# Kernel tuning notes

Measured on AMD Instinct MI355X. Metric: run time of the kernel, lower is better.

Reference implementation:

```python
import jax, jax.numpy as jnp
import numpy as np

N_NODES = 100000
N_EDGES = 1600000
GENE_DIM = 256
HID = 128
NUM_CLASSES = 2
BN_EPS = 1e-5


def setup_inputs() -> dict:
    key = jax.random.key(0)
    ks = jax.random.split(key, 24)
    g = lambda k, shape, scale: (jax.random.normal(k, shape, dtype=jnp.float32) * scale)
    inp = {
        "x": g(ks[0], (N_NODES, GENE_DIM), 1.0),
        "edge_index": jax.random.randint(ks[1], (2, N_EDGES), 0, N_NODES, dtype=jnp.int64),
        # GCNConv weights (glorot-ish scale) and biases
        "W1": g(ks[2], (GENE_DIM, HID), 1.0 / np.sqrt(GENE_DIM)), "b1": jnp.zeros((HID,), jnp.float32),
        "W2": g(ks[3], (HID, 2 * HID), 1.0 / np.sqrt(HID)), "b2": jnp.zeros((2 * HID,), jnp.float32),
        "W3": g(ks[4], (2 * HID, HID), 1.0 / np.sqrt(2 * HID)), "b3": jnp.zeros((HID,), jnp.float32),
        "W4": g(ks[5], (HID, HID // 2), 1.0 / np.sqrt(HID)), "b4": jnp.zeros((HID // 2,), jnp.float32),
        "Wc": g(ks[6], (HID // 2, NUM_CLASSES), 1.0 / np.sqrt(HID // 2)), "bc": jnp.zeros((NUM_CLASSES,), jnp.float32),
        # BatchNorm affine params
        "g1": jnp.ones((HID,), jnp.float32), "be1": jnp.zeros((HID,), jnp.float32),
        "g2": jnp.ones((2 * HID,), jnp.float32), "be2": jnp.zeros((2 * HID,), jnp.float32),
        "g3": jnp.ones((HID,), jnp.float32), "be3": jnp.zeros((HID,), jnp.float32),
        "g4": jnp.ones((HID // 2,), jnp.float32), "be4": jnp.zeros((HID // 2,), jnp.float32),
    }
    return inp


def _batchnorm(h, gamma, beta):
    # training-mode BatchNorm1d: per-feature batch stats (biased variance)
    mean = h.mean(axis=0)
    var = ((h - mean) ** 2).mean(axis=0)
    return gamma * (h - mean) * jax.lax.rsqrt(var + BN_EPS) + beta


def _gcn_conv(h, W, b, src, dst, norm, n):
    # PyG GCNConv: linear transform, then sym-normalized aggregation over
    # edges (self-loops already included in src/dst/norm), then bias.
    m = h @ W                                   # [n, d_out]
    msg = m[src] * norm[:, None]                # [E+n, d_out] gather
    agg = jax.ops.segment_sum(msg, dst, num_segments=n)  # scatter-add
    return agg + b


def reference(x, edge_index, W1, b1, W2, b2, W3, b3, W4, b4, Wc, bc,
              g1, be1, g2, be2, g3, be3, g4, be4):
    n = x.shape[0]
    loop = jnp.arange(n, dtype=edge_index.dtype)
    src = jnp.concatenate([edge_index[0], loop])  # add self-loops
    dst = jnp.concatenate([edge_index[1], loop])
    deg = jax.ops.segment_sum(jnp.ones_like(dst, dtype=x.dtype), dst, num_segments=n)
    dinv = jax.lax.rsqrt(jnp.maximum(deg, 1.0))
    norm = dinv[src] * dinv[dst]                  # D^-1/2 (A+I) D^-1/2

    h = jax.nn.relu(_gcn_conv(x, W1, b1, src, dst, norm, n))
    h = _batchnorm(h, g1, be1)
    h = jax.nn.relu(_gcn_conv(h, W2, b2, src, dst, norm, n))
    h = _batchnorm(h, g2, be2)
    h = jax.nn.relu(_gcn_conv(h, W3, b3, src, dst, norm, n))
    h = _batchnorm(h, g3, be3)
    out4 = jax.nn.relu(_gcn_conv(h, W4, b4, src, dst, norm, n))
    bn4 = _batchnorm(out4, g4, be4)
    logits = bn4 @ Wc + bc
    return (logits, out4, bn4)
```

## Files before the change

### kernel.cpp

```cpp
#include <hip/hip_runtime.h>
#include <hip/hip_bf16.h>

#define N_NODES 100000
#define N_EDGES 1600000
#define NB ((N_NODES + 255) / 256)
#define CHUNK 16384
#define NBLK ((N_EDGES + CHUNK - 1) / CHUNK)
#define NSHADOW 32
#define WCB 416
#define SB 512

typedef short sh8 __attribute__((ext_vector_type(8)));
typedef float f32x4 __attribute__((ext_vector_type(4)));

__device__ __forceinline__ float bf2f(unsigned short s) {
    return __uint_as_float(((unsigned int)s) << 16);
}
__device__ __forceinline__ unsigned short f2bf(float f) {
    unsigned int u = __float_as_uint(f);
    unsigned int r = (u + 0x7FFFu + ((u >> 16) & 1u)) >> 16;
    return (unsigned short)r;
}
__device__ __forceinline__ float blo(unsigned int u) { return __uint_as_float(u << 16); }
__device__ __forceinline__ float bhi(unsigned int u) { return __uint_as_float(u & 0xffff0000u); }


__global__ __launch_bounds__(256) void k_hist(const int* __restrict__ ei, int* __restrict__ histG) {
    __shared__ int hist[NB];
    int blk = blockIdx.x, t = threadIdx.x;
    for (int b = t; b < NB; b += 256) hist[b] = 0;
    __syncthreads();
    int e0 = blk * CHUNK;
    int e1 = min(e0 + CHUNK, N_EDGES);
    for (int e = e0 + t; e < e1; e += 256) atomicAdd(&hist[ei[N_EDGES + e] >> 8], 1);
    __syncthreads();
    for (int b = t; b < NB; b += 256) histG[b * NBLK + blk] = hist[b];
}

__global__ __launch_bounds__(128) void k_scanrow(int* __restrict__ histG, int* __restrict__ rowsum) {
    __shared__ int sm[128];
    int b = blockIdx.x, t = threadIdx.x;
    int v = (t < NBLK) ? histG[b * NBLK + t] : 0;
    sm[t] = v; __syncthreads();
    for (int d = 1; d < 128; d <<= 1) {
        int add = (t >= d) ? sm[t - d] : 0;
        __syncthreads(); sm[t] += add; __syncthreads();
    }
    if (t < NBLK) histG[b * NBLK + t] = sm[t] - v;
    if (t == 127) rowsum[b] = sm[127];
}

__global__ __launch_bounds__(512) void k_scanbkt(const int* __restrict__ rowsum, int* __restrict__ rowbase) {
    __shared__ int sm[512];
    int t = threadIdx.x;
    int v = (t < NB) ? rowsum[t] : 0;
    sm[t] = v; __syncthreads();
    for (int d = 1; d < 512; d <<= 1) {
        int add = (t >= d) ? sm[t - d] : 0;
        __syncthreads(); sm[t] += add; __syncthreads();
    }
    if (t <= NB) rowbase[t] = sm[t] - v;
}

__global__ __launch_bounds__(256) void k_part(const int* __restrict__ ei, const int* __restrict__ histG,
                                              const int* __restrict__ rowbase, unsigned* __restrict__ pairs) {
    __shared__ int cur[NB];
    int blk = blockIdx.x, t = threadIdx.x;
    for (int b = t; b < NB; b += 256) cur[b] = rowbase[b] + histG[b * NBLK + blk];
    __syncthreads();
    int e0 = blk * CHUNK;
    int e1 = min(e0 + CHUNK, N_EDGES);
    for (int e = e0 + t; e < e1; e += 256) {
        int s = ei[e], d = ei[N_EDGES + e];
        int pos = atomicAdd(&cur[d >> 8], 1);
        pairs[pos] = ((unsigned)s << 8) | (unsigned)(d & 255);
    }
}

__global__ __launch_bounds__(256) void k_bsort(const unsigned* __restrict__ pairs, const int* __restrict__ rowbase,
                                               int* __restrict__ col, int* __restrict__ basep,
                                               int* __restrict__ deg, float* __restrict__ dinv,
                                               float* __restrict__ sdeg) {
    __shared__ int cnt[256];
    __shared__ int sm[256];
    __shared__ int cur[256];
    int b = blockIdx.x, t = threadIdx.x;
    int base = rowbase[b], end = rowbase[b + 1];
    cnt[t] = 0; __syncthreads();
    for (int e = base + t; e < end; e += 256) atomicAdd(&cnt[pairs[e] & 255], 1);
    __syncthreads();
    int v = cnt[t];
    sm[t] = v; __syncthreads();
    for (int d = 1; d < 256; d <<= 1) {
        int add = (t >= d) ? sm[t - d] : 0;
        __syncthreads(); sm[t] += add; __syncthreads();
    }
    int excl = sm[t] - v;
    cur[t] = excl;
    int gd = (b << 8) + t;
    if (gd < N_NODES) {
        basep[gd] = base + excl;
        deg[gd] = v;
        dinv[gd] = rsqrtf((float)(v + 1));
        sdeg[gd] = sqrtf((float)(v + 1));
    }
    __syncthreads();
    for (int e = base + t; e < end; e += 256) {
        unsigned p = pairs[e];
        int pos = atomicAdd(&cur[p & 255], 1);
        col[base + pos] = (int)(p >> 8);
    }
}


__global__ __launch_bounds__(256) void k_wsvec(const float* __restrict__ W1, const float* __restrict__ W2,
                                               const float* __restrict__ W3, const float* __restrict__ W4,
                                               unsigned short* __restrict__ Wt1, unsigned short* __restrict__ Wt2,
                                               unsigned short* __restrict__ Wt3, unsigned short* __restrict__ Wt4,
                                               const int* __restrict__ col, const int* __restrict__ basep,
                                               const int* __restrict__ deg, const float* __restrict__ dinv,
                                               float* __restrict__ svec) {
    if (blockIdx.x < WCB) {
        int idx = blockIdx.x * 256 + threadIdx.x;
        const float* W; unsigned short* Wt; int K, N, base;
        if (idx < 32768)       { W = W1; Wt = Wt1; K = 256; N = 128; base = 0; }
        else if (idx < 65536)  { W = W2; Wt = Wt2; K = 128; N = 256; base = 32768; }
        else if (idx < 98304)  { W = W3; Wt = Wt3; K = 256; N = 128; base = 65536; }
        else if (idx < 106496) { W = W4; Wt = Wt4; K = 128; N = 64;  base = 98304; }
        else return;
        int li = idx - base;
        int n = li / K, k = li - n * K;
        Wt[li] = f2bf(W[(size_t)k * N + n]);
        return;
    }
    int sb = blockIdx.x - WCB;
    int w = (sb * 256 + threadIdx.x) >> 6;
    if (w >= N_NODES) return;
    int lane = threadIdx.x & 63;
    int start = basep[w], cnt = deg[w];
    float s = 0.f;
    for (int j = lane; j < cnt; j += 64) s += dinv[col[start + j]];
#pragma unroll
    for (int off = 32; off; off >>= 1) s += __shfl_down(s, off, 64);
    if (lane == 0) { float di = dinv[w]; svec[w] = di * (s + di); }
}


__global__ __launch_bounds__(256) void k_bnred(const float* __restrict__ arena, float* __restrict__ dst) {
    int f = blockIdx.x * 256 + threadIdx.x;
    float s = 0.f;
#pragma unroll
    for (int i = 0; i < NSHADOW; ++i) s += arena[i * 512 + f];
    dst[f] = s;
}


template <int D, bool INF32, bool RESCALE>
__device__ __forceinline__ void bnstats_body(int bid, int gridN, const void* __restrict__ h,
                                             const float* __restrict__ sdeg, float* __restrict__ arena) {
    constexpr int VEC = INF32 ? 4 : 8;
    constexpr int TPR = D / VEC;
    constexpr int RPB = 256 / TPR;
    const int tid = threadIdx.x;
    const int rg = tid / TPR;
    const int oc = tid % TPR;
    const int fb = oc * VEC;

    float s1[VEC], s2[VEC];
#pragma unroll
    for (int k = 0; k < VEC; ++k) { s1[k] = 0.f; s2[k] = 0.f; }

    for (int r = bid * RPB + rg; r < N_NODES; r += gridN * RPB) {
        float rs = 1.f;
        if constexpr (RESCALE) rs = sdeg[r];
        if constexpr (INF32) {
            float4 v = *(const float4*)((const float*)h + (size_t)r * D + fb);
            float vv[4] = {v.x, v.y, v.z, v.w};
#pragma unroll
            for (int k = 0; k < 4; ++k) {
                float val = vv[k];
                if constexpr (RESCALE) val *= rs;
                s1[k] += val; s2[k] += val * val;
            }
        } else {
            uint4 u = *(const uint4*)((const unsigned short*)h + (size_t)r * D + fb);
            unsigned uu[4] = {u.x, u.y, u.z, u.w};
#pragma unroll
            for (int k = 0; k < 4; ++k) {
                float v0 = blo(uu[k]), v1 = bhi(uu[k]);
                if constexpr (RESCALE) { v0 *= rs; v1 *= rs; }
                s1[2 * k] += v0;     s2[2 * k] += v0 * v0;
                s1[2 * k + 1] += v1; s2[2 * k + 1] += v1 * v1;
            }
        }
    }

    __shared__ float red[2][D];
    for (int i = tid; i < 2 * D; i += 256) ((float*)red)[i] = 0.f;
    __syncthreads();
#pragma unroll
    for (int k = 0; k < VEC; ++k) {
        atomicAdd(&red[0][fb + k], s1[k]);
        atomicAdd(&red[1][fb + k], s2[k]);
    }
    __syncthreads();
    float* slot = arena + ((bid & (NSHADOW - 1)) << 9);
    for (int i = tid; i < 2 * D; i += 256) {
        int f = (i < D) ? i : (256 + i - D);
        float v = (i < D) ? red[0][i] : red[1][i - D];
        atomicAdd(&slot[f], v);
    }
}

template <int D, bool INF32, bool RESCALE>
__global__ __launch_bounds__(256) void k_bnstats(const void* __restrict__ h,
                                                 const float* __restrict__ sdeg,
                                                 float* __restrict__ arena) {
    bnstats_body<D, INF32, RESCALE>(blockIdx.x, gridDim.x, h, sdeg, arena);
}


template <int D, bool PRE, bool OUTF32, bool OUTSCALE>
__device__ __forceinline__ void agg_body(int bid, const unsigned short* __restrict__ m,
                                         const int* __restrict__ col,
                                         const int* __restrict__ basep,
                                         const int* __restrict__ deg,
                                         const float* __restrict__ dinv,
                                         const float* __restrict__ bias,
                                         void* __restrict__ out) {
    constexpr int VPL = D / 64;
    const int w = (bid * 256 + threadIdx.x) >> 6;
    if (w >= N_NODES) return;
    const int lane = threadIdx.x & 63;
    const int fo = lane * VPL;
    const unsigned short* mfo = m + fo;
    float acc[VPL];
#pragma unroll
    for (int k = 0; k < VPL; ++k) acc[k] = 0.f;

    int start = basep[w], cnt = deg[w];
    int j = 0;
    for (; j + 8 <= cnt; j += 8) {
        int sx[8];
#pragma unroll
        for (int i = 0; i < 8; ++i) sx[i] = col[start + j + i];
        if constexpr (VPL == 2) {
            unsigned u[8];
#pragma unroll
            for (int i = 0; i < 8; ++i) u[i] = *(const unsigned*)(mfo + (size_t)sx[i] * D);
#pragma unroll
            for (int i = 0; i < 8; ++i) { acc[0] += blo(u[i]); acc[1] += bhi(u[i]); }
        } else {
            float v[8];
#pragma unroll
            for (int i = 0; i < 8; ++i) v[i] = bf2f(mfo[(size_t)sx[i] * D]);
#pragma unroll
            for (int i = 0; i < 8; ++i) acc[0] += v[i];
        }
    }
    for (; j < cnt; ++j) {
        int s0 = col[start + j];
        if constexpr (VPL == 2) {
            unsigned u0 = *(const unsigned*)(mfo + (size_t)s0 * D);
            acc[0] += blo(u0); acc[1] += bhi(u0);
        } else {
            acc[0] += bf2f(mfo[(size_t)s0 * D]);
        }
    }
    if constexpr (VPL == 2) {
        unsigned u0 = *(const unsigned*)(mfo + (size_t)w * D);
        acc[0] += blo(u0); acc[1] += bhi(u0);
    } else {
        acc[0] += bf2f(mfo[(size_t)w * D]);
    }

    float di = dinv[w];
    float o[VPL];
    if constexpr (PRE) {
#pragma unroll
        for (int k = 0; k < VPL; ++k) o[k] = acc[k] * di;
    } else {
#pragma unroll
        for (int k = 0; k < VPL; ++k) {
            o[k] = fmaxf(acc[k] * di + bias[fo + k], 0.f);
            if constexpr (OUTSCALE) o[k] *= di;
        }
    }

    if constexpr (OUTF32) {
        float* of = (float*)out;
#pragma unroll
        for (int k = 0; k < VPL; ++k) of[(size_t)w * D + fo + k] = o[k];
    } else {
        unsigned short* ob = (unsigned short*)out + (size_t)w * D + fo;
        if constexpr (VPL == 2) {
            unsigned int u = (unsigned)f2bf(o[0]) | ((unsigned)f2bf(o[1]) << 16);
            *(unsigned int*)ob = u;
        } else {
            ob[0] = f2bf(o[0]);
        }
    }
}

template <int D, bool PRE, bool OUTF32, bool OUTSCALE>
__global__ __launch_bounds__(256) void k_agg(const unsigned short* __restrict__ m,
                                             const int* __restrict__ col,
                                             const int* __restrict__ basep,
                                             const int* __restrict__ deg,
                                             const float* __restrict__ dinv,
                                             const float* __restrict__ bias,
                                             void* __restrict__ out) {
    agg_body<D, PRE, OUTF32, OUTSCALE>(blockIdx.x, m, col, basep, deg, dinv, bias, out);
}


__global__ __launch_bounds__(256) void k_aggpre_stats(const unsigned short* __restrict__ hb,
                                                      const int* __restrict__ col,
                                                      const int* __restrict__ basep,
                                                      const int* __restrict__ deg,
                                                      const float* __restrict__ dinv,
                                                      const float* __restrict__ sdeg,
                                                      unsigned short* __restrict__ mb,
                                                      float* __restrict__ arena) {
    if (blockIdx.x < SB) {
        bnstats_body<128, false, true>(blockIdx.x, SB, hb, sdeg, arena);
    } else {
        agg_body<128, true, false, false>(blockIdx.x - SB, hb, col, basep, deg, dinv, nullptr, mb);
    }
}


template <bool OUTF32>
__global__ __launch_bounds__(256) void k_agg64(const unsigned short* __restrict__ m,
                                               const int* __restrict__ col,
                                               const int* __restrict__ basep,
                                               const int* __restrict__ deg,
                                               const float* __restrict__ dinv,
                                               const float* __restrict__ bias,
                                               void* __restrict__ out) {
    const int w = (blockIdx.x * 256 + threadIdx.x) >> 5;
    if (w >= N_NODES) return;
    const int hl = threadIdx.x & 31;
    const int fo = hl * 2;
    const unsigned short* mfo = m + fo;
    float acc0 = 0.f, acc1 = 0.f;

    int start = basep[w], cnt = deg[w];
    int j = 0;
    for (; j + 8 <= cnt; j += 8) {
        int sx[8];
#pragma unroll
        for (int i = 0; i < 8; ++i) sx[i] = col[start + j + i];
        unsigned u[8];
#pragma unroll
        for (int i = 0; i < 8; ++i) u[i] = *(const unsigned*)(mfo + (size_t)sx[i] * 64);
#pragma unroll
        for (int i = 0; i < 8; ++i) { acc0 += blo(u[i]); acc1 += bhi(u[i]); }
    }
    for (; j < cnt; ++j) {
        int s0 = col[start + j];
        unsigned u0 = *(const unsigned*)(mfo + (size_t)s0 * 64);
        acc0 += blo(u0); acc1 += bhi(u0);
    }
    {
        unsigned u0 = *(const unsigned*)(mfo + (size_t)w * 64);
        acc0 += blo(u0); acc1 += bhi(u0);
    }

    float di = dinv[w];
    float o0 = fmaxf(acc0 * di + bias[fo], 0.f);
    float o1 = fmaxf(acc1 * di + bias[fo + 1], 0.f);

    if constexpr (OUTF32) {
        *(float2*)((float*)out + (size_t)w * 64 + fo) = make_float2(o0, o1);
    } else {
        unsigned u = (unsigned)f2bf(o0) | ((unsigned)f2bf(o1) << 16);
        *(unsigned*)((unsigned short*)out + (size_t)w * 64 + fo) = u;
    }
}


template <int BM, int BN, int AMODE, bool BIASRELU, bool DSCALE>
__global__ __launch_bounds__(512) void k_gemm4(const void* __restrict__ Ain,
                                               const unsigned short* __restrict__ Wt,
                                               const float* __restrict__ arena,
                                               const float* __restrict__ gamma,
                                               const float* __restrict__ beta,
                                               const float* __restrict__ svec,
                                               const float* __restrict__ bias,
                                               const float* __restrict__ dinv,
                                               unsigned short* __restrict__ Mout,
                                               int K, int NTOT) {
    constexpr int BK = 64;
    constexpr int LDA = 72;
    constexpr int AP = BM / 64;
    constexpr int BP = BN / 64;
    constexpr int MF = BM / 32;
    constexpr int NF = BN / 64;
    __shared__ unsigned short As[BM * LDA];
    __shared__ unsigned short Bs[BN * LDA];
    __shared__ float ss_sc[256];
    __shared__ float ss_sh[256];
    const int tid = threadIdx.x;
    const int lane = tid & 63;
    const int wv = tid >> 6;
    const int wm = wv >> 2;
    const int wn = wv & 3;
    const int row0 = blockIdx.x * BM;
    const int col0 = blockIdx.y * BN;

    if constexpr (AMODE >= 1) {
        for (int f = tid; f < K; f += 512) {
            float s1 = 0.f, s2 = 0.f;
#pragma unroll
            for (int s = 0; s < NSHADOW; ++s) {
                s1 += arena[s * 512 + f];
                s2 += arena[s * 512 + 256 + f];
            }
            float mean = s1 * (1.f / N_NODES);
            float var = s2 * (1.f / N_NODES) - mean * mean;
            float inv = rsqrtf(var + 1e-5f);
            float sc = gamma[f] * inv;
            ss_sc[f] = sc;
            ss_sh[f] = beta[f] - mean * sc;
        }
        __syncthreads();
    }

    const int sr = tid >> 3;
    const int scc = (tid & 7) * 8;

    float4 fa[AP][2];
    uint4 ua[AP];
    uint4 ub[BP];
    float sv[AP];

    auto LOAD = [&](int k0) {
#pragma unroll
        for (int p = 0; p < AP; ++p) {
            int gr = row0 + p * 64 + sr;
            if constexpr (AMODE == 0) {
                const float* Af = (const float*)Ain;
                fa[p][0] = make_float4(0.f, 0.f, 0.f, 0.f); fa[p][1] = fa[p][0];
                if (gr < N_NODES) {
                    const float* p0 = Af + (size_t)gr * K + k0 + scc;
                    fa[p][0] = *(const float4*)p0;
                    fa[p][1] = *(const float4*)(p0 + 4);
                }
            } else {
                const unsigned short* Ab = (const unsigned short*)Ain;
                ua[p] = make_uint4(0, 0, 0, 0);
                if (gr < N_NODES) ua[p] = *(const uint4*)(Ab + (size_t)gr * K + k0 + scc);
                if constexpr (AMODE == 2) sv[p] = (gr < N_NODES) ? svec[gr] : 0.f;
            }
        }
#pragma unroll
        for (int p = 0; p < BP; ++p)
            ub[p] = *(const uint4*)(Wt + (size_t)(col0 + p * 64 + sr) * K + k0 + scc);
    };

    auto WRITE = [&](int k0) {
#pragma unroll
        for (int p = 0; p < AP; ++p) {
            alignas(16) unsigned short tmp[8];
            if constexpr (AMODE == 0) {
                tmp[0] = f2bf(fa[p][0].x); tmp[1] = f2bf(fa[p][0].y);
                tmp[2] = f2bf(fa[p][0].z); tmp[3] = f2bf(fa[p][0].w);
                tmp[4] = f2bf(fa[p][1].x); tmp[5] = f2bf(fa[p][1].y);
                tmp[6] = f2bf(fa[p][1].z); tmp[7] = f2bf(fa[p][1].w);
            } else {
                const unsigned short* pr = (const unsigned short*)&ua[p];
#pragma unroll
                for (int q = 0; q < 8; ++q) {
                    float sc = ss_sc[k0 + scc + q];
                    float sh = ss_sh[k0 + scc + q];
                    float val;
                    if constexpr (AMODE == 2) val = bf2f(pr[q]) * sc + sh * sv[p];
                    else val = bf2f(pr[q]) * sc + sh;
                    tmp[q] = f2bf(val);
                }
            }
            *(uint4*)&As[(p * 64 + sr) * LDA + scc] = *(const uint4*)tmp;
        }
#pragma unroll
        for (int p = 0; p < BP; ++p) *(uint4*)&Bs[(p * 64 + sr) * LDA + scc] = ub[p];
    };

    f32x4 acc[MF][NF];
#pragma unroll
    for (int i = 0; i < MF; ++i)
#pragma unroll
        for (int j = 0; j < NF; ++j)
#pragma unroll
            for (int r = 0; r < 4; ++r) acc[i][j][r] = 0.f;

    LOAD(0);
    WRITE(0);
    __syncthreads();
    const int nk = K / BK;
    for (int kt = 1; kt <= nk; ++kt) {
        if (kt < nk) LOAD(kt * BK);
#pragma unroll
        for (int ks = 0; ks < 2; ++ks) {
            sh8 af[MF], bfr[NF];
#pragma unroll
            for (int i = 0; i < MF; ++i)
                af[i] = *(const sh8*)&As[(wm * (BM / 2) + i * 16 + (lane & 15)) * LDA + ks * 32 + (lane >> 4) * 8];
#pragma unroll
            for (int j = 0; j < NF; ++j)
                bfr[j] = *(const sh8*)&Bs[(wn * NF * 16 + j * 16 + (lane & 15)) * LDA + ks * 32 + (lane >> 4) * 8];
#pragma unroll
            for (int i = 0; i < MF; ++i)
#pragma unroll
                for (int j = 0; j < NF; ++j)
                    acc[i][j] = __builtin_amdgcn_mfma_f32_16x16x32_bf16(af[i], bfr[j], acc[i][j], 0, 0, 0);
        }
        __syncthreads();
        if (kt < nk) {
            WRITE(kt * BK);
            __syncthreads();
        }
    }

#pragma unroll
    for (int i = 0; i < MF; ++i) {
#pragma unroll
        for (int r = 0; r < 4; ++r) {
            int grow = row0 + wm * (BM / 2) + i * 16 + (lane >> 4) * 4 + r;
            if (grow >= N_NODES) continue;
            float rsc = 1.f;
            if constexpr (DSCALE) rsc = dinv[grow];
#pragma unroll
            for (int j = 0; j < NF; ++j) {
                int gcol = col0 + wn * NF * 16 + j * 16 + (lane & 15);
                float v = acc[i][j][r];
                if constexpr (BIASRELU) v = fmaxf(v + bias[gcol], 0.f);
                if constexpr (DSCALE) v *= rsc;
                Mout[(size_t)grow * NTOT + gcol] = f2bf(v);
            }
        }
    }
}


__global__ __launch_bounds__(256) void k_bnlog(const float* __restrict__ out4, const float* __restrict__ sums,
                                               const float* __restrict__ gamma, const float* __restrict__ beta,
                                               const float* __restrict__ Wc, const float* __restrict__ bc,
                                               float* __restrict__ bn4, float* __restrict__ logits) {
    int gw = (blockIdx.x * 256 + threadIdx.x) >> 6;
    if (gw >= N_NODES) return;
    int f = threadIdx.x & 63;
    float mean = sums[f] * (1.f / N_NODES);
    float var = sums[256 + f] * (1.f / N_NODES) - mean * mean;
    float inv = rsqrtf(var + 1e-5f);
    float sc = gamma[f] * inv;
    float sh = beta[f] - mean * sc;
    float v = out4[(size_t)gw * 64 + f];
    float bn = v * sc + sh;
    bn4[(size_t)gw * 64 + f] = bn;
    float a0 = bn * Wc[2 * f];
    float a1 = bn * Wc[2 * f + 1];
#pragma unroll
    for (int off = 32; off; off >>= 1) {
        a0 += __shfl_down(a0, off, 64);
        a1 += __shfl_down(a1, off, 64);
    }
    if (f == 0) {
        logits[2 * gw] = a0 + bc[0];
        logits[2 * gw + 1] = a1 + bc[1];
    }
}


extern "C" void kernel_launch(void* const* d_in, const int* in_sizes, int n_in,
                              void* d_out, int out_size, void* d_ws, size_t ws_size,
                              hipStream_t stream) {
    const float* x  = (const float*)d_in[0];
    const int* ei   = (const int*)d_in[1];
    const float* W1 = (const float*)d_in[2];  const float* b1  = (const float*)d_in[3];
    const float* W2 = (const float*)d_in[4];  const float* b2  = (const float*)d_in[5];
    const float* W3 = (const float*)d_in[6];  const float* b3  = (const float*)d_in[7];
    const float* W4 = (const float*)d_in[8];  const float* b4  = (const float*)d_in[9];
    const float* Wc = (const float*)d_in[10]; const float* bc  = (const float*)d_in[11];
    const float* g1 = (const float*)d_in[12]; const float* be1 = (const float*)d_in[13];
    const float* g2 = (const float*)d_in[14]; const float* be2 = (const float*)d_in[15];
    const float* g3 = (const float*)d_in[16]; const float* be3 = (const float*)d_in[17];
    const float* g4 = (const float*)d_in[18]; const float* be4 = (const float*)d_in[19];

    char* wsb = (char*)d_ws;
    size_t off = 0;
    auto alloc = [&](size_t bytes) -> void* {
        void* p = wsb + off;
        off = (off + bytes + 511) & ~(size_t)511;
        return p;
    };
    int* deg     = (int*)alloc((size_t)N_NODES * 4);
    int* basep   = (int*)alloc((size_t)N_NODES * 4);
    float* dinv  = (float*)alloc((size_t)N_NODES * 4);
    float* sdeg  = (float*)alloc((size_t)N_NODES * 4);
    float* svec  = (float*)alloc((size_t)N_NODES * 4);
    int* col     = (int*)alloc((size_t)N_EDGES * 4);
    unsigned* pairs = (unsigned*)alloc((size_t)N_EDGES * 4);
    int* histG   = (int*)alloc((size_t)NB * NBLK * 4);
    int* rowsum  = (int*)alloc((size_t)NB * 4);
    int* rowbase = (int*)alloc((size_t)(NB + 1) * 4);
    float* sums4  = (float*)alloc(512 * 4);
    float* shadow = (float*)alloc((size_t)4 * NSHADOW * 512 * 4);
    unsigned short* Wt1 = (unsigned short*)alloc((size_t)256 * 128 * 2);
    unsigned short* Wt2 = (unsigned short*)alloc((size_t)128 * 256 * 2);
    unsigned short* Wt3 = (unsigned short*)alloc((size_t)256 * 128 * 2);
    unsigned short* Wt4 = (unsigned short*)alloc((size_t)128 * 64 * 2);
    unsigned short* mb = (unsigned short*)alloc((size_t)N_NODES * 128 * 2);
    unsigned short* hb = (unsigned short*)alloc((size_t)N_NODES * 256 * 2);

    float* arena1 = shadow;
    float* arena2 = shadow + NSHADOW * 512;
    float* arena3 = shadow + 2 * NSHADOW * 512;
    float* arena4 = shadow + 3 * NSHADOW * 512;

    float* outLogits = (float*)d_out;
    float* out4 = outLogits + (size_t)N_NODES * 2;
    float* bn4  = out4 + (size_t)N_NODES * 64;

    hipMemsetAsync(sums4, 0, 512 * 4 + (size_t)4 * NSHADOW * 512 * 4, stream);

    k_hist<<<NBLK, 256, 0, stream>>>(ei, histG);
    k_scanrow<<<NB, 128, 0, stream>>>(histG, rowsum);
    k_scanbkt<<<1, 512, 0, stream>>>(rowsum, rowbase);
    k_part<<<NBLK, 256, 0, stream>>>(ei, histG, rowbase, pairs);
    k_bsort<<<NB, 256, 0, stream>>>(pairs, rowbase, col, basep, deg, dinv, sdeg);
    k_wsvec<<<WCB + (N_NODES + 3) / 4, 256, 0, stream>>>(W1, W2, W3, W4, Wt1, Wt2, Wt3, Wt4,
                                                         col, basep, deg, dinv, svec);

    const int GB128 = (N_NODES + 127) / 128;
    const int GB64  = (N_NODES + 63) / 64;
    const int AB = (N_NODES + 3) / 4;
    const int HB = (N_NODES + 7) / 8;

    k_gemm4<128, 128, 0, false, true><<<dim3(GB128, 1), 512, 0, stream>>>(
        x, Wt1, nullptr, nullptr, nullptr, nullptr, nullptr, dinv, mb, 256, 128);
    k_agg<128, false, false, true><<<AB, 256, 0, stream>>>(
        mb, col, basep, deg, dinv, b1, hb);

    k_aggpre_stats<<<SB + AB, 256, 0, stream>>>(hb, col, basep, deg, dinv, sdeg, mb, arena1);

    k_gemm4<128, 128, 2, true, false><<<dim3(GB128, 2), 512, 0, stream>>>(
        mb, Wt2, arena1, g1, be1, svec, b2, nullptr, hb, 128, 256);
    k_bnstats<256, false, false><<<SB, 256, 0, stream>>>(hb, nullptr, arena2);

    k_gemm4<128, 128, 1, false, true><<<dim3(GB128, 1), 512, 0, stream>>>(
        hb, Wt3, arena2, g2, be2, nullptr, nullptr, dinv, mb, 256, 128);
    k_agg<128, false, false, false><<<AB, 256, 0, stream>>>(
        mb, col, basep, deg, dinv, b3, hb);
    k_bnstats<128, false, false><<<SB, 256, 0, stream>>>(hb, nullptr, arena3);

    k_gemm4<64, 64, 1, false, true><<<dim3(GB64, 1), 512, 0, stream>>>(
        hb, Wt4, arena3, g3, be3, nullptr, nullptr, dinv, mb, 128, 64);
    k_agg64<true><<<HB, 256, 0, stream>>>(
        mb, col, basep, deg, dinv, b4, out4);
    k_bnstats<64, true, false><<<SB, 256, 0, stream>>>(out4, nullptr, arena4);
    k_bnred<<<2, 256, 0, stream>>>(arena4, sums4);
    k_bnlog<<<(N_NODES * 64 + 255) / 256, 256, 0, stream>>>(out4, sums4, g4, be4, Wc, bc, bn4, outLogits);
}
```

Measured before the change: 588.2 us.

## Fuse BN stats into layer-2 GEMM epilogue and merge small prep kernels

Adds a STATS mode to the GEMM epilogue that accumulates per-column sum and sum-of-squares. These are reduced in shared memory and added atomically into shadow arena slots, which removes the separate bnstats pass that re-read the 100000x256 layer-2 output. The weight transpose and bf16 conversion are folded into the histogram kernel, and the svec computation moves into the first aggregation launch, cutting two launches. The cost is extra global atomics per GEMM block and more register pressure in the GEMM epilogue.

After: 581.7 us. No clear change (-1.1%).

```diff
diff --git a/kernel.cpp b/kernel.cpp
--- a/kernel.cpp
+++ b/kernel.cpp
@@ -25,16 +25,33 @@
 __device__ __forceinline__ float bhi(unsigned int u) { return __uint_as_float(u & 0xffff0000u); }
 
 
-__global__ __launch_bounds__(256) void k_hist(const int* __restrict__ ei, int* __restrict__ histG) {
-    __shared__ int hist[NB];
-    int blk = blockIdx.x, t = threadIdx.x;
-    for (int b = t; b < NB; b += 256) hist[b] = 0;
-    __syncthreads();
-    int e0 = blk * CHUNK;
-    int e1 = min(e0 + CHUNK, N_EDGES);
-    for (int e = e0 + t; e < e1; e += 256) atomicAdd(&hist[ei[N_EDGES + e] >> 8], 1);
-    __syncthreads();
-    for (int b = t; b < NB; b += 256) histG[b * NBLK + blk] = hist[b];
+__global__ __launch_bounds__(256) void k_hist_wconv(const int* __restrict__ ei, int* __restrict__ histG,
+                                                    const float* __restrict__ W1, const float* __restrict__ W2,
+                                                    const float* __restrict__ W3, const float* __restrict__ W4,
+                                                    unsigned short* __restrict__ Wt1, unsigned short* __restrict__ Wt2,
+                                                    unsigned short* __restrict__ Wt3, unsigned short* __restrict__ Wt4) {
+    if (blockIdx.x < NBLK) {
+        __shared__ int hist[NB];
+        int blk = blockIdx.x, t = threadIdx.x;
+        for (int b = t; b < NB; b += 256) hist[b] = 0;
+        __syncthreads();
+        int e0 = blk * CHUNK;
+        int e1 = min(e0 + CHUNK, N_EDGES);
+        for (int e = e0 + t; e < e1; e += 256) atomicAdd(&hist[ei[N_EDGES + e] >> 8], 1);
+        __syncthreads();
+        for (int b = t; b < NB; b += 256) histG[b * NBLK + blk] = hist[b];
+        return;
+    }
+    int idx = (blockIdx.x - NBLK) * 256 + threadIdx.x;
+    const float* W; unsigned short* Wt; int K, N, base;
+    if (idx < 32768)       { W = W1; Wt = Wt1; K = 256; N = 128; base = 0; }
+    else if (idx < 65536)  { W = W2; Wt = Wt2; K = 128; N = 256; base = 32768; }
+    else if (idx < 98304)  { W = W3; Wt = Wt3; K = 256; N = 128; base = 65536; }
+    else if (idx < 106496) { W = W4; Wt = Wt4; K = 128; N = 64;  base = 98304; }
+    else return;
+    int li = idx - base;
+    int n = li / K, k = li - n * K;
+    Wt[li] = f2bf(W[(size_t)k * N + n]);
 }
 
 __global__ __launch_bounds__(128) void k_scanrow(int* __restrict__ histG, int* __restrict__ rowsum) {
@@ -113,39 +130,6 @@
 }
 
 
-__global__ __launch_bounds__(256) void k_wsvec(const float* __restrict__ W1, const float* __restrict__ W2,
-                                               const float* __restrict__ W3, const float* __restrict__ W4,
-                                               unsigned short* __restrict__ Wt1, unsigned short* __restrict__ Wt2,
-                                               unsigned short* __restrict__ Wt3, unsigned short* __restrict__ Wt4,
-                                               const int* __restrict__ col, const int* __restrict__ basep,
-                                               const int* __restrict__ deg, const float* __restrict__ dinv,
-                                               float* __restrict__ svec) {
-    if (blockIdx.x < WCB) {
-        int idx = blockIdx.x * 256 + threadIdx.x;
-        const float* W; unsigned short* Wt; int K, N, base;
-        if (idx < 32768)       { W = W1; Wt = Wt1; K = 256; N = 128; base = 0; }
-        else if (idx < 65536)  { W = W2; Wt = Wt2; K = 128; N = 256; base = 32768; }
-        else if (idx < 98304)  { W = W3; Wt = Wt3; K = 256; N = 128; base = 65536; }
-        else if (idx < 106496) { W = W4; Wt = Wt4; K = 128; N = 64;  base = 98304; }
-        else return;
-        int li = idx - base;
-        int n = li / K, k = li - n * K;
-        Wt[li] = f2bf(W[(size_t)k * N + n]);
-        return;
-    }
-    int sb = blockIdx.x - WCB;
-    int w = (sb * 256 + threadIdx.x) >> 6;
-    if (w >= N_NODES) return;
-    int lane = threadIdx.x & 63;
-    int start = basep[w], cnt = deg[w];
-    float s = 0.f;
-    for (int j = lane; j < cnt; j += 64) s += dinv[col[start + j]];
-#pragma unroll
-    for (int off = 32; off; off >>= 1) s += __shfl_down(s, off, 64);
-    if (lane == 0) { float di = dinv[w]; svec[w] = di * (s + di); }
-}
-
-
 __global__ __launch_bounds__(256) void k_bnred(const float* __restrict__ arena, float* __restrict__ dst) {
     int f = blockIdx.x * 256 + threadIdx.x;
     float s = 0.f;
@@ -314,6 +298,31 @@
 }
 
 
+__global__ __launch_bounds__(256) void k_agg_svec(const unsigned short* __restrict__ m,
+                                                  const int* __restrict__ col,
+                                                  const int* __restrict__ basep,
+                                                  const int* __restrict__ deg,
+                                                  const float* __restrict__ dinv,
+                                                  const float* __restrict__ bias,
+                                                  unsigned short* __restrict__ out,
+                                                  float* __restrict__ svec, int AB) {
+    if (blockIdx.x < (unsigned)AB) {
+        agg_body<128, false, false, true>(blockIdx.x, m, col, basep, deg, dinv, bias, out);
+        return;
+    }
+    int sb = blockIdx.x - AB;
+    int w = (sb * 256 + threadIdx.x) >> 6;
+    if (w >= N_NODES) return;
+    int lane = threadIdx.x & 63;
+    int start = basep[w], cnt = deg[w];
+    float s = 0.f;
+    for (int j = lane; j < cnt; j += 64) s += dinv[col[start + j]];
+#pragma unroll
+    for (int off = 32; off; off >>= 1) s += __shfl_down(s, off, 64);
+    if (lane == 0) { float di = dinv[w]; svec[w] = di * (s + di); }
+}
+
+
 __global__ __launch_bounds__(256) void k_aggpre_stats(const unsigned short* __restrict__ hb,
                                                       const int* __restrict__ col,
                                                       const int* __restrict__ basep,
@@ -380,7 +389,7 @@
 }
 
 
-template <int BM, int BN, int AMODE, bool BIASRELU, bool DSCALE>
+template <int BM, int BN, int AMODE, bool BIASRELU, bool DSCALE, bool STATS>
 __global__ __launch_bounds__(512) void k_gemm4(const void* __restrict__ Ain,
                                                const unsigned short* __restrict__ Wt,
                                                const float* __restrict__ arena,
@@ -390,6 +399,7 @@
                                                const float* __restrict__ bias,
                                                const float* __restrict__ dinv,
                                                unsigned short* __restrict__ Mout,
+                                               float* __restrict__ arena_out,
                                                int K, int NTOT) {
     constexpr int BK = 64;
     constexpr int LDA = 72;
@@ -522,6 +532,11 @@
         }
     }
 
+    float cs[NF], cs2[NF];
+    if constexpr (STATS) {
+#pragma unroll
+        for (int j = 0; j < NF; ++j) { cs[j] = 0.f; cs2[j] = 0.f; }
+    }
 #pragma unroll
     for (int i = 0; i < MF; ++i) {
 #pragma unroll
@@ -536,8 +551,26 @@
                 float v = acc[i][j][r];
                 if constexpr (BIASRELU) v = fmaxf(v + bias[gcol], 0.f);
                 if constexpr (DSCALE) v *= rsc;
+                if constexpr (STATS) { cs[j] += v; cs2[j] += v * v; }
                 Mout[(size_t)grow * NTOT + gcol] = f2bf(v);
             }
+        }
+    }
+    if constexpr (STATS) {
+        __shared__ float red[2][BN];
+        for (int i = tid; i < 2 * BN; i += 512) ((float*)red)[i] = 0.f;
+        __syncthreads();
+#pragma unroll
+        for (int j = 0; j < NF; ++j) {
+            int lc = wn * NF * 16 + j * 16 + (lane & 15);
+            atomicAdd(&red[0][lc], cs[j]);
+            atomicAdd(&red[1][lc], cs2[j]);
+        }
+        __syncthreads();
+        float* slot = arena_out + ((blockIdx.x & (NSHADOW - 1)) << 9);
+        for (int f = tid; f < BN; f += 512) {
+            atomicAdd(&slot[col0 + f], red[0][f]);
+            atomicAdd(&slot[256 + col0 + f], red[1][f]);
         }
     }
 }
@@ -624,38 +657,35 @@
 
     hipMemsetAsync(sums4, 0, 512 * 4 + (size_t)4 * NSHADOW * 512 * 4, stream);
 
-    k_hist<<<NBLK, 256, 0, stream>>>(ei, histG);
+    k_hist_wconv<<<NBLK + WCB, 256, 0, stream>>>(ei, histG, W1, W2, W3, W4, Wt1, Wt2, Wt3, Wt4);
     k_scanrow<<<NB, 128, 0, stream>>>(histG, rowsum);
     k_scanbkt<<<1, 512, 0, stream>>>(rowsum, rowbase);
     k_part<<<NBLK, 256, 0, stream>>>(ei, histG, rowbase, pairs);
     k_bsort<<<NB, 256, 0, stream>>>(pairs, rowbase, col, basep, deg, dinv, sdeg);
-    k_wsvec<<<WCB + (N_NODES + 3) / 4, 256, 0, stream>>>(W1, W2, W3, W4, Wt1, Wt2, Wt3, Wt4,
-                                                         col, basep, deg, dinv, svec);
 
     const int GB128 = (N_NODES + 127) / 128;
     const int GB64  = (N_NODES + 63) / 64;
     const int AB = (N_NODES + 3) / 4;
     const int HB = (N_NODES + 7) / 8;
 
-    k_gemm4<128, 128, 0, false, true><<<dim3(GB128, 1), 512, 0, stream>>>(
-        x, Wt1, nullptr, nullptr, nullptr, nullptr, nullptr, dinv, mb, 256, 128);
-    k_agg<128, false, false, true><<<AB, 256, 0, stream>>>(
-        mb, col, basep, deg, dinv, b1, hb);
+    k_gemm4<128, 128, 0, false, true, false><<<dim3(GB128, 1), 512, 0, stream>>>(
+        x, Wt1, nullptr, nullptr, nullptr, nullptr, nullptr, dinv, mb, nullptr, 256, 128);
+    k_agg_svec<<<AB + AB, 256, 0, stream>>>(
+        mb, col, basep, deg, dinv, b1, hb, svec, AB);
 
     k_aggpre_stats<<<SB + AB, 256, 0, stream>>>(hb, col, basep, deg, dinv, sdeg, mb, arena1);
 
-    k_gemm4<128, 128, 2, true, false><<<dim3(GB128, 2), 512, 0, stream>>>(
-        mb, Wt2, arena1, g1, be1, svec, b2, nullptr, hb, 128, 256);
-    k_bnstats<256, false, false><<<SB, 256, 0, stream>>>(hb, nullptr, arena2);
-
-    k_gemm4<128, 128, 1, false, true><<<dim3(GB128, 1), 512, 0, stream>>>(
-        hb, Wt3, arena2, g2, be2, nullptr, nullptr, dinv, mb, 256, 128);
+    k_gemm4<128, 128, 2, true, false, true><<<dim3(GB128, 2), 512, 0, stream>>>(
+        mb, Wt2, arena1, g1, be1, svec, b2, nullptr, hb, arena2, 128, 256);
+
+    k_gemm4<128, 128, 1, false, true, false><<<dim3(GB128, 1), 512, 0, stream>>>(
+        hb, Wt3, arena2, g2, be2, nullptr, nullptr, dinv, mb, nullptr, 256, 128);
     k_agg<128, false, false, false><<<AB, 256, 0, stream>>>(
         mb, col, basep, deg, dinv, b3, hb);
     k_bnstats<128, false, false><<<SB, 256, 0, stream>>>(hb, nullptr, arena3);
 
-    k_gemm4<64, 64, 1, false, true><<<dim3(GB64, 1), 512, 0, stream>>>(
-        hb, Wt4, arena3, g3, be3, nullptr, nullptr, dinv, mb, 128, 64);
+    k_gemm4<64, 64, 1, false, true, false><<<dim3(GB64, 1), 512, 0, stream>>>(
+        hb, Wt4, arena3, g3, be3, nullptr, nullptr, dinv, mb, nullptr, 128, 64);
     k_agg64<true><<<HB, 256, 0, stream>>>(
         mb, col, basep, deg, dinv, b4, out4);
     k_bnstats<64, true, false><<<SB, 256, 0, stream>>>(out4, nullptr, arena4);
```
